# Kernel tuning notes

Measured on AMD Instinct MI355X. Metric: run time of the kernel, lower is better.

## Reference

```python
import jax, jax.numpy as jnp
import numpy as np
import math

D_MODEL = 1024
N_HEADS = 16
HEAD_DIM = D_MODEL // N_HEADS
THETA = 10000.0


def _rope(x, cos, sin):
    # x: [b, h, s, head_dim]; cos/sin: [s, head_dim//2]
    xe = x[..., 0::2]
    xo = x[..., 1::2]
    re = xe * cos - xo * sin
    ro = xe * sin + xo * cos
    # interleave back to even/odd layout
    return jnp.stack([re, ro], axis=-1).reshape(x.shape)


def setup_inputs() -> dict:
    key = jax.random.key(0)
    k1, k2, k3, k4, k5 = jax.random.split(key, 5)
    std = math.sqrt(2.0 / (D_MODEL + D_MODEL))
    x = jax.random.normal(k1, (2, 2048, D_MODEL), dtype=jnp.float32)
    Wq = jax.random.normal(k2, (D_MODEL, D_MODEL), dtype=jnp.float32) * std
    Wk = jax.random.normal(k3, (D_MODEL, D_MODEL), dtype=jnp.float32) * std
    Wv = jax.random.normal(k4, (D_MODEL, D_MODEL), dtype=jnp.float32) * std
    Wo = jax.random.normal(k5, (D_MODEL, D_MODEL), dtype=jnp.float32) * (std / math.sqrt(2))
    return {"x": x, "Wq": Wq, "Wk": Wk, "Wv": Wv, "Wo": Wo}


def reference(x, Wq, Wk, Wv, Wo):
    b, s, d = x.shape
    h, hd = N_HEADS, HEAD_DIM
    # projections: einsum 'batch seq d_in, d_model d_in -> batch seq d_model' == x @ W.T
    def proj(W):
        y = jnp.einsum('bsd,md->bsm', x, W)
        return y.reshape(b, s, h, hd).transpose(0, 2, 1, 3)  # [b, h, s, hd]
    Q, K, V = proj(Wq), proj(Wk), proj(Wv)
    # RoPE with default positions = arange(seq)
    freqs = 1.0 / (THETA ** (jnp.arange(0, hd, 2, dtype=jnp.float32) / hd))
    angles = jnp.arange(s, dtype=jnp.float32)[:, None] * freqs[None, :]  # [s, hd//2]
    cos, sin = jnp.cos(angles), jnp.sin(angles)
    Q = _rope(Q, cos, sin)
    K = _rope(K, cos, sin)
    # naive causal attention
    scores = jnp.einsum('bhqd,bhkd->bhqk', Q, K) / math.sqrt(hd)
    causal = jnp.tril(jnp.ones((s, s), dtype=bool))
    scores = jnp.where(causal, scores, -jnp.inf)
    attn = jax.nn.softmax(scores, axis=-1)
    out = jnp.einsum('bhqk,bhkd->bhqd', attn, V)
    out = out.transpose(0, 2, 1, 3).reshape(b, s, d)
    return jnp.einsum('bsd,md->bsm', out, Wo)
```

## Files before the change

### kernel.cpp

```cpp
#include <hip/hip_runtime.h>
#include <stdint.h>
#include <stddef.h>

typedef __bf16 bf16;
typedef __bf16 bf16x8 __attribute__((ext_vector_type(8)));
typedef __bf16 bf16x4 __attribute__((ext_vector_type(4)));
typedef short short4v __attribute__((ext_vector_type(4)));
typedef float f32x4 __attribute__((ext_vector_type(4)));

#define GAS __attribute__((address_space(1)))
#define LAS __attribute__((address_space(3)))

__device__ __forceinline__ void async_load16(const void* g, void* l) {
  __builtin_amdgcn_global_load_lds((const GAS void*)g, (LAS void*)l, 16, 0, 0);
}

__device__ __forceinline__ f32x4 mfma16(bf16x4 a, bf16x4 b, f32x4 c) {
#if defined(__HIP_DEVICE_COMPILE__)
#if __has_builtin(__builtin_amdgcn_mfma_f32_16x16x16bf16_1k)
  return __builtin_amdgcn_mfma_f32_16x16x16bf16_1k(
      __builtin_bit_cast(short4v, a), __builtin_bit_cast(short4v, b), c, 0, 0, 0);
#else
  f32x4 d;
  asm volatile("v_mfma_f32_16x16x16_bf16 %0, %1, %2, %3"
               : "=v"(d)
               : "v"(a), "v"(b), "v"(c));
  return d;
#endif
#else
  (void)a; (void)b;
  return c;
#endif
}

__global__ __launch_bounds__(256) void cast_all(
    const float* __restrict__ x, const float* __restrict__ Wq,
    const float* __restrict__ Wk, const float* __restrict__ Wv,
    const float* __restrict__ Wo, bf16* __restrict__ Xh,
    bf16* __restrict__ Wqkv, bf16* __restrict__ Woh,
    float2* __restrict__ rope) {
  if (blockIdx.x >= 8192) {
    const int e = ((blockIdx.x - 8192) * 256 + threadIdx.x) * 4;
    const int s = e >> 5, ip0 = e & 31;
#pragma unroll
    for (int r = 0; r < 4; ++r) {
      const float freq = __expf((float)(ip0 + r) * -0.2878231366242557f);
      float sn, cs;
      __sincosf((float)s * freq, &sn, &cs);
      rope[e + r] = make_float2(cs, sn);
    }
    return;
  }
  int idx = (blockIdx.x * 256 + threadIdx.x) * 4;
  const float* src;
  bf16* dst;
  float scale = 1.0f;
  if (idx < 4194304) {
    src = x + idx; dst = Xh + idx;
  } else if (idx < 7340032) {
    int j = idx - 4194304;
    if (j < 1048576) {
      src = Wq + j; scale = 0.18033688011112042f;
    } else {
      src = ((j < 2097152) ? Wk : Wv) + (j & 1048575);
    }
    dst = Wqkv + j;
  } else {
    int j = idx - 7340032;
    src = Wo + j; dst = Woh + j;
  }
  float4 v = *(const float4*)src;
  bf16x4 o;
  o[0] = (bf16)(v.x * scale); o[1] = (bf16)(v.y * scale);
  o[2] = (bf16)(v.z * scale); o[3] = (bf16)(v.w * scale);
  *(bf16x4*)dst = o;
}

__global__ __launch_bounds__(256, 3) void gemm_qkv(
    const bf16* __restrict__ A, const bf16* __restrict__ B,
    const float2* __restrict__ rope, bf16* __restrict__ Qh,
    bf16* __restrict__ Kh, bf16* __restrict__ Vt, int K) {
  __shared__ __align__(16) bf16 As[128 * 64];
  __shared__ __align__(16) bf16 Bs[128 * 64];
  const int tid = threadIdx.x;
  const int wave = tid >> 6, lane = tid & 63;
  const int bm = blockIdx.y * 128, bn = blockIdx.x * 128;
  const int wm = (wave >> 1) * 64, wn = (wave & 1) * 64;
  const int fr = lane & 15, g = lane >> 4;
  const int sw8 = (fr & 7) * 8;

  const int srow = tid >> 3;
  const int scol = 8 * ((tid & 7) ^ (srow & 7));
  const int ldst = wave * 512;

  f32x4 acc[4][4] = {};

  for (int kt = 0; kt < K; kt += 64) {
    __syncthreads();
#pragma unroll
    for (int s = 0; s < 4; ++s) {
      const int row = s * 32 + srow;
      async_load16(A + (size_t)(bm + row) * K + kt + scol,
                   (void*)(As + s * 2048 + ldst));
      async_load16(B + (size_t)(bn + row) * K + kt + scol,
                   (void*)(Bs + s * 2048 + ldst));
    }
    __syncthreads();

#pragma unroll
    for (int ks = 0; ks < 2; ++ks) {
      bf16x8 af[4], bfr[4];
      const int kq = (ks * 32 + g * 8) ^ sw8;
#pragma unroll
      for (int i = 0; i < 4; ++i)
        af[i] = *(const bf16x8*)&As[(wm + i * 16 + fr) * 64 + kq];
#pragma unroll
      for (int j = 0; j < 4; ++j)
        bfr[j] = *(const bf16x8*)&Bs[(wn + j * 16 + fr) * 64 + kq];
#pragma unroll
      for (int i = 0; i < 4; ++i)
#pragma unroll
        for (int j = 0; j < 4; ++j)
          acc[i][j] = __builtin_amdgcn_mfma_f32_16x16x32_bf16(af[i], bfr[j],
                                                              acc[i][j], 0, 0, 0);
    }
  }

  const int r0 = (lane >> 4) * 4, cc = lane & 15;
  const bool oddl = cc & 1;
#pragma unroll
  for (int i = 0; i < 4; ++i) {
    const int row0 = bm + wm + i * 16 + r0;
    const int b = row0 >> 11, s0 = row0 & 2047;
#pragma unroll
    for (int j = 0; j < 4; ++j) {
      const int col = bn + wn + j * 16 + cc;
      if (col < 2048) {
        const int hcol = col & 1023;
        const int h = hcol >> 6, d = hcol & 63;
        const int ip = d >> 1;
        const bool isK = col >= 1024;
        bf16* dst = (isK ? Kh : Qh) + ((size_t)(b * 16 + h) * 2048) * 64;
#pragma unroll
        for (int r = 0; r < 4; ++r) {
          float own = acc[i][j][r];
          float oth = __shfl_xor(own, 1, 64);
          const float2 t = rope[((s0 + r) << 5) + ip];
          float res = oddl ? (oth * t.y + own * t.x) : (own * t.x - oth * t.y);
          dst[(size_t)(s0 + r) * 64 + d] = (bf16)res;
        }
      } else {
        const int v = col - 2048, h = v >> 6, d = v & 63;
        bf16x4 o;
#pragma unroll
        for (int r = 0; r < 4; ++r) o[r] = (bf16)acc[i][j][r];
        const int s2 = (s0 & ~63) | ((s0 ^ ((d & 7) << 3)) & 63);
        *(bf16x4*)&Vt[(((size_t)b * 16 + h) * 64 + d) * 2048 + s2] = o;
      }
    }
  }
}

template <typename OutT, int BM, int BN>
__global__ __launch_bounds__(256) void gemm_bt(
    const bf16* __restrict__ A, const bf16* __restrict__ B,
    OutT* __restrict__ C, int M, int N, int K) {
  constexpr int FM = BM / 32, FN = BN / 32;
  constexpr int SA = BM / 32, SB = BN / 32;
  __shared__ __align__(16) bf16 As[BM * 64];
  __shared__ __align__(16) bf16 Bs[BN * 64];
  const int tid = threadIdx.x;
  const int wave = tid >> 6, lane = tid & 63;
  const int bm = blockIdx.y * BM, bn = blockIdx.x * BN;
  const int wm = (wave >> 1) * (BM / 2), wn = (wave & 1) * (BN / 2);
  const int fr = lane & 15, g = lane >> 4;
  const int sw8 = (fr & 7) * 8;
  const int srow = tid >> 3;
  const int scol = 8 * ((tid & 7) ^ (srow & 7));
  const int ldst = wave * 512;

  f32x4 acc[FM][FN] = {};

  for (int kt = 0; kt < K; kt += 64) {
    __syncthreads();
#pragma unroll
    for (int s = 0; s < SA; ++s)
      async_load16(A + (size_t)(bm + s * 32 + srow) * K + kt + scol,
                   (void*)(As + s * 2048 + ldst));
#pragma unroll
    for (int s = 0; s < SB; ++s)
      async_load16(B + (size_t)(bn + s * 32 + srow) * K + kt + scol,
                   (void*)(Bs + s * 2048 + ldst));
    __syncthreads();

#pragma unroll
    for (int ks = 0; ks < 2; ++ks) {
      const int kq = (ks * 32 + g * 8) ^ sw8;
      bf16x8 af[FM], bfr[FN];
#pragma unroll
      for (int i = 0; i < FM; ++i)
        af[i] = *(const bf16x8*)&As[(wm + i * 16 + fr) * 64 + kq];
#pragma unroll
      for (int j = 0; j < FN; ++j)
        bfr[j] = *(const bf16x8*)&Bs[(wn + j * 16 + fr) * 64 + kq];
#pragma unroll
      for (int i = 0; i < FM; ++i)
#pragma unroll
        for (int j = 0; j < FN; ++j)
          acc[i][j] = __builtin_amdgcn_mfma_f32_16x16x32_bf16(af[i], bfr[j],
                                                              acc[i][j], 0, 0, 0);
    }
  }

  const int r0 = (lane >> 4) * 4, cc = lane & 15;
#pragma unroll
  for (int i = 0; i < FM; ++i)
#pragma unroll
    for (int j = 0; j < FN; ++j)
#pragma unroll
      for (int r = 0; r < 4; ++r)
        C[(size_t)(bm + wm + i * 16 + r0 + r) * N + (bn + wn + j * 16 + cc)] =
            (OutT)acc[i][j][r];
}

__global__ __launch_bounds__(128, 2) void attn(const bf16* __restrict__ Qh,
                                               const bf16* __restrict__ Kh,
                                               const bf16* __restrict__ Vt,
                                               bf16* __restrict__ Oh) {
  __shared__ __align__(16) bf16 Vs[2][2][64 * 64];
  const int f = blockIdx.x;
  const int bh = f & 31;
  const int P = (f >> 5) & 31;
  const int tid = threadIdx.x, w = tid >> 6, lane = tid & 63;
  const int nlo = lane & 15, g = lane >> 4;
  const bf16* __restrict__ Qp = Qh + (size_t)bh * 131072;
  const bf16* __restrict__ Kp = Kh + (size_t)bh * 131072;
  const bf16* __restrict__ Vp = Vt + (size_t)bh * 131072;
  const int bb = bh >> 4, hd = bh & 15;
  const int sw = (nlo & 7) << 3;
  const int srow = lane >> 3, soff = (lane & 7) * 8;
  bf16* __restrict__ Vw0 = Vs[w][0];
  bf16* __restrict__ Vw1 = Vs[w][1];
  float* __restrict__ scr = (float*)Vs[1][0];
  float* __restrict__ scl = (float*)Vs[1][1];

  bf16x8 pkA[4][2], pkB[4][2];

  for (int ph = 0; ph < 2; ++ph) {
    const int qt = ph ? P : 63 - P;
    const int q0 = qt * 32;
    const int n = (qt >> 1) + 1;
    const int h = (n + 1) >> 1;
    const int t0 = w ? h : 0;
    const int cnt = w ? (n - h) : h;

    bf16x8 aq[2][2];
#pragma unroll
    for (int qb = 0; qb < 2; ++qb)
#pragma unroll
      for (int ks = 0; ks < 2; ++ks)
        aq[qb][ks] = *(const bf16x8*)&Qp[(size_t)(q0 + qb * 16 + nlo) * 64 +
                                         ks * 32 + g * 8];

    f32x4 oacc[2][4] = {};
    float lsum[2] = {0.f, 0.f};

    auto ldK = [&](bf16x8 (&pk)[4][2], int i) {
#pragma unroll
      for (int ni = 0; ni < 4; ++ni)
#pragma unroll
        for (int ks = 0; ks < 2; ++ks)
          pk[ni][ks] = *(const bf16x8*)&Kp[(size_t)(i * 64 + ni * 16 + nlo) * 64 +
                                           ks * 32 + g * 8];
    };
    auto stageV = [&](bf16* dst, int i) {
      const bf16* src = Vp + (size_t)srow * 2048 + i * 64 + soff;
#pragma unroll
      for (int c = 0; c < 8; ++c)
        async_load16(src + (size_t)c * 16384, (void*)(dst + c * 512));
    };

    auto body = [&](int it, bf16x8 (&pkC)[4][2], bf16x8 (&pkN)[4][2],
                    bf16* VwC, bf16* VwN) {
      const int i = t0 + it;
      asm volatile("s_waitcnt vmcnt(8)" ::: "memory");
      f32x4 st[2][4] = {};
#pragma unroll
      for (int qb = 0; qb < 2; ++qb)
#pragma unroll
        for (int ks = 0; ks < 2; ++ks)
#pragma unroll
          for (int ni = 0; ni < 4; ++ni)
            st[qb][ni] = __builtin_amdgcn_mfma_f32_16x16x32_bf16(
                pkC[ni][ks], aq[qb][ks], st[qb][ni], 0, 0, 0);
      const bool more = (it + 1 < cnt);
      if (more) {
        ldK(pkN, i + 1);
        stageV(VwN, i + 1);
      }
      const int kbase = i * 64;
      const bool dg = (i == n - 1);
      bf16x4 p[2][4];
#pragma unroll
      for (int qb = 0; qb < 2; ++qb) {
        const int qg = q0 + qb * 16 + nlo;
        if (!dg) {
#pragma unroll
          for (int ni = 0; ni < 4; ++ni)
#pragma unroll
            for (int r = 0; r < 4; ++r) {
              float e = __builtin_amdgcn_exp2f(st[qb][ni][r]);
              lsum[qb] += e;
              p[qb][ni][r] = (bf16)e;
            }
        } else {
#pragma unroll
          for (int ni = 0; ni < 4; ++ni) {
            const int kg0 = kbase + ni * 16 + g * 4;
#pragma unroll
            for (int r = 0; r < 4; ++r) {
              float e = __builtin_amdgcn_exp2f(st[qb][ni][r]);
              e = (kg0 + r <= qg) ? e : 0.0f;
              lsum[qb] += e;
              p[qb][ni][r] = (bf16)e;
            }
          }
        }
      }
      if (more)
        asm volatile("s_waitcnt vmcnt(16)" ::: "memory");
      else
        asm volatile("s_waitcnt vmcnt(0)" ::: "memory");
#pragma unroll
      for (int ni = 0; ni < 4; ++ni)
#pragma unroll
        for (int mi = 0; mi < 4; ++mi) {
          bf16x4 av = *(const bf16x4*)&VwC[(mi * 16 + nlo) * 64 +
                                           ((ni * 16 + g * 4) ^ sw)];
#pragma unroll
          for (int qb = 0; qb < 2; ++qb)
            oacc[qb][mi] = mfma16(av, p[qb][ni], oacc[qb][mi]);
        }
    };

    if (cnt > 0) {
      ldK(pkA, t0);
      stageV(Vw0, t0);
      int it = 0;
      while (true) {
        body(it, pkA, pkB, Vw0, Vw1);
        if (++it >= cnt) break;
        body(it, pkB, pkA, Vw1, Vw0);
        if (++it >= cnt) break;
      }
    }

#pragma unroll
    for (int qb = 0; qb < 2; ++qb) {
      lsum[qb] += __shfl_xor(lsum[qb], 16, 64);
      lsum[qb] += __shfl_xor(lsum[qb], 32, 64);
    }

    if (w == 1) {
#pragma unroll
      for (int qb = 0; qb < 2; ++qb) {
#pragma unroll
        for (int mi = 0; mi < 4; ++mi)
#pragma unroll
          for (int r = 0; r < 4; ++r)
            scr[(qb * 16 + mi * 4 + r) * 64 + lane] = oacc[qb][mi][r];
        scl[qb * 64 + lane] = lsum[qb];
      }
    }
    __syncthreads();
    if (w == 0) {
#pragma unroll
      for (int qb = 0; qb < 2; ++qb) {
        const float l = lsum[qb] + scl[qb * 64 + lane];
        const float inv = 1.0f / l;
        const int q = q0 + qb * 16 + nlo;
#pragma unroll
        for (int mi = 0; mi < 4; ++mi) {
          bf16x4 o;
#pragma unroll
          for (int r = 0; r < 4; ++r)
            o[r] = (bf16)((oacc[qb][mi][r] +
                           scr[(qb * 16 + mi * 4 + r) * 64 + lane]) * inv);
          *(bf16x4*)&Oh[((size_t)bb * 2048 + q) * 1024 + hd * 64 + mi * 16 +
                        g * 4] = o;
        }
      }
    }
    __syncthreads();
  }
}

extern "C" void kernel_launch(void* const* d_in, const int* in_sizes, int n_in,
                              void* d_out, int out_size, void* d_ws, size_t ws_size,
                              hipStream_t stream) {
  (void)in_sizes; (void)n_in; (void)out_size; (void)ws_size;
  const float* x = (const float*)d_in[0];
  const float* Wq = (const float*)d_in[1];
  const float* Wk = (const float*)d_in[2];
  const float* Wv = (const float*)d_in[3];
  const float* Wo = (const float*)d_in[4];
  float* out = (float*)d_out;
  char* ws = (char*)d_ws;

  bf16* Xh    = (bf16*)(ws);
  bf16* Wqkv  = (bf16*)(ws + 8388608);
  bf16* Woh   = (bf16*)(ws + 14680064);
  bf16* Qh    = (bf16*)(ws + 16777216);
  bf16* Kh    = (bf16*)(ws + 25165824);
  bf16* Vt    = (bf16*)(ws + 33554432);
  bf16* Oh    = (bf16*)(ws + 41943040);
  float2* rope = (float2*)(ws + 50331648);

  cast_all<<<8256, 256, 0, stream>>>(x, Wq, Wk, Wv, Wo, Xh, Wqkv, Woh, rope);
  gemm_qkv<<<dim3(24, 32), 256, 0, stream>>>(Xh, Wqkv, rope, Qh, Kh, Vt, 1024);
  attn<<<1024, 128, 0, stream>>>(Qh, Kh, Vt, Oh);
  gemm_bt<float, 128, 128><<<dim3(8, 32), 256, 0, stream>>>(Oh, Woh, out, 4096, 1024, 1024);
}
```

Measured before the change: 183.1 us.

## Software-pipeline attention loop: overlap PV of tile i with QK/exp of tile i+1

Restructures the per-wave KV loop into a skewed pipeline: each iteration runs the PV MFMAs for the current tile, issues the V stage for the next tile and a K prefetch two tiles ahead, then computes QK and exp for the next tile. This is meant to hide exp/VALU latency and load waits behind MFMA work, and it adds s_setprio around the MFMA blocks. It also adds a __syncthreads before the cross-wave reduction. The vmcnt accounting and the final V buffer selection are more intricate and could be fragile.

```diff
diff --git a/kernel.cpp b/kernel.cpp
--- a/kernel.cpp
+++ b/kernel.cpp
@@ -264,6 +264,8 @@
 
     f32x4 oacc[2][4] = {};
     float lsum[2] = {0.f, 0.f};
+    f32x4 st[2][4];
+    bf16x4 p[2][4];
 
     auto ldK = [&](bf16x8 (&pk)[4][2], int i) {
 #pragma unroll
@@ -279,28 +281,22 @@
       for (int c = 0; c < 8; ++c)
         async_load16(src + (size_t)c * 16384, (void*)(dst + c * 512));
     };
-
-    auto body = [&](int it, bf16x8 (&pkC)[4][2], bf16x8 (&pkN)[4][2],
-                    bf16* VwC, bf16* VwN) {
-      const int i = t0 + it;
-      asm volatile("s_waitcnt vmcnt(8)" ::: "memory");
-      f32x4 st[2][4] = {};
-#pragma unroll
-      for (int qb = 0; qb < 2; ++qb)
+    auto qk = [&](bf16x8 (&pk)[4][2]) {
+#pragma unroll
+      for (int qb = 0; qb < 2; ++qb) {
+#pragma unroll
+        for (int ni = 0; ni < 4; ++ni) st[qb][ni] = f32x4{0.f, 0.f, 0.f, 0.f};
 #pragma unroll
         for (int ks = 0; ks < 2; ++ks)
 #pragma unroll
           for (int ni = 0; ni < 4; ++ni)
             st[qb][ni] = __builtin_amdgcn_mfma_f32_16x16x32_bf16(
-                pkC[ni][ks], aq[qb][ks], st[qb][ni], 0, 0, 0);
-      const bool more = (it + 1 < cnt);
-      if (more) {
-        ldK(pkN, i + 1);
-        stageV(VwN, i + 1);
-      }
+                pk[ni][ks], aq[qb][ks], st[qb][ni], 0, 0, 0);
+      }
+    };
+    auto expv = [&](int i) {
       const int kbase = i * 64;
       const bool dg = (i == n - 1);
-      bf16x4 p[2][4];
 #pragma unroll
       for (int qb = 0; qb < 2; ++qb) {
         const int qg = q0 + qb * 16 + nlo;
@@ -327,32 +323,63 @@
           }
         }
       }
-      if (more)
-        asm volatile("s_waitcnt vmcnt(16)" ::: "memory");
-      else
-        asm volatile("s_waitcnt vmcnt(0)" ::: "memory");
+    };
+    auto pv = [&](const bf16* Vw) {
 #pragma unroll
       for (int ni = 0; ni < 4; ++ni)
 #pragma unroll
         for (int mi = 0; mi < 4; ++mi) {
-          bf16x4 av = *(const bf16x4*)&VwC[(mi * 16 + nlo) * 64 +
-                                           ((ni * 16 + g * 4) ^ sw)];
+          bf16x4 av = *(const bf16x4*)&Vw[(mi * 16 + nlo) * 64 +
+                                          ((ni * 16 + g * 4) ^ sw)];
 #pragma unroll
           for (int qb = 0; qb < 2; ++qb)
             oacc[qb][mi] = mfma16(av, p[qb][ni], oacc[qb][mi]);
         }
     };
 
+    auto body = [&](int it, bf16x8 (&pkQK)[4][2], bf16x8 (&pkPre)[4][2],
+                    bf16* VwC, bf16* VwN) {
+      const int i = t0 + it;
+      asm volatile("s_waitcnt vmcnt(8)" ::: "memory");
+      __builtin_amdgcn_s_setprio(1);
+      pv(VwC);
+      __builtin_amdgcn_s_setprio(0);
+      stageV(VwN, i + 1);
+      const bool preK = (it + 2 < cnt);
+      if (preK) ldK(pkPre, i + 2);
+      if (preK)
+        asm volatile("s_waitcnt vmcnt(16)" ::: "memory");
+      else
+        asm volatile("s_waitcnt vmcnt(8)" ::: "memory");
+      __builtin_amdgcn_s_setprio(1);
+      qk(pkQK);
+      __builtin_amdgcn_s_setprio(0);
+      expv(i + 1);
+    };
+
     if (cnt > 0) {
       ldK(pkA, t0);
       stageV(Vw0, t0);
+      if (cnt > 1) ldK(pkB, t0 + 1);
+      if (cnt > 1)
+        asm volatile("s_waitcnt vmcnt(16)" ::: "memory");
+      else
+        asm volatile("s_waitcnt vmcnt(8)" ::: "memory");
+      qk(pkA);
+      expv(t0);
+
       int it = 0;
-      while (true) {
-        body(it, pkA, pkB, Vw0, Vw1);
-        if (++it >= cnt) break;
-        body(it, pkB, pkA, Vw1, Vw0);
-        if (++it >= cnt) break;
-      }
+      while (it + 1 < cnt) {
+        body(it, pkB, pkA, Vw0, Vw1);
+        ++it;
+        if (it + 1 >= cnt) break;
+        body(it, pkA, pkB, Vw1, Vw0);
+        ++it;
+      }
+
+      asm volatile("s_waitcnt vmcnt(0)" ::: "memory");
+      pv((cnt & 1) ? ((cnt == 1) ? Vw0 : ((cnt - 1) & 1 ? Vw1 : Vw0))
+                   : Vw1);
     }
 
 #pragma unroll
@@ -361,6 +388,7 @@
       lsum[qb] += __shfl_xor(lsum[qb], 32, 64);
     }
 
+    __syncthreads();
     if (w == 1) {
 #pragma unroll
       for (int qb = 0; qb < 2; ++qb) {
```

New measurement: 204.0 us. +11.4%, slower.

## Single-buffer attention V staging and launch one query tile per block

Applied to the files above, without the earlier changes.

The attention kernel no longer pairs a long and a short query tile in one block. It launches 2048 blocks, one 32-row query tile each, ordered longest first. The V tile in LDS and the K register fragments are now single-buffered, which halves LDS per block, and launch bounds are raised to four blocks per SM. Prefetch of the next V tile only starts after the current tile's PV MFMAs, so less load latency is hidden per block; the design relies on higher occupancy to cover it.

```diff
diff --git a/kernel.cpp b/kernel.cpp
--- a/kernel.cpp
+++ b/kernel.cpp
@@ -223,175 +223,154 @@
             (OutT)acc[i][j][r];
 }
 
-__global__ __launch_bounds__(128, 2) void attn(const bf16* __restrict__ Qh,
+__global__ __launch_bounds__(128, 4) void attn(const bf16* __restrict__ Qh,
                                                const bf16* __restrict__ Kh,
                                                const bf16* __restrict__ Vt,
                                                bf16* __restrict__ Oh) {
-  __shared__ __align__(16) bf16 Vs[2][2][64 * 64];
+  __shared__ __align__(16) bf16 Vs[2][4096];
   const int f = blockIdx.x;
+  const int qt = 63 - (f >> 5);
   const int bh = f & 31;
-  const int P = (f >> 5) & 31;
   const int tid = threadIdx.x, w = tid >> 6, lane = tid & 63;
   const int nlo = lane & 15, g = lane >> 4;
+  const int q0 = qt * 32;
   const bf16* __restrict__ Qp = Qh + (size_t)bh * 131072;
   const bf16* __restrict__ Kp = Kh + (size_t)bh * 131072;
   const bf16* __restrict__ Vp = Vt + (size_t)bh * 131072;
+  const int n = (qt >> 1) + 1;
+  const int h = (n + 1) >> 1;
+  const int t0 = w ? h : 0;
+  const int cnt = w ? (n - h) : h;
   const int bb = bh >> 4, hd = bh & 15;
   const int sw = (nlo & 7) << 3;
   const int srow = lane >> 3, soff = (lane & 7) * 8;
-  bf16* __restrict__ Vw0 = Vs[w][0];
-  bf16* __restrict__ Vw1 = Vs[w][1];
-  float* __restrict__ scr = (float*)Vs[1][0];
-  float* __restrict__ scl = (float*)Vs[1][1];
-
-  bf16x8 pkA[4][2], pkB[4][2];
-
-  for (int ph = 0; ph < 2; ++ph) {
-    const int qt = ph ? P : 63 - P;
-    const int q0 = qt * 32;
-    const int n = (qt >> 1) + 1;
-    const int h = (n + 1) >> 1;
-    const int t0 = w ? h : 0;
-    const int cnt = w ? (n - h) : h;
-
-    bf16x8 aq[2][2];
-#pragma unroll
-    for (int qb = 0; qb < 2; ++qb)
+  bf16* __restrict__ Vw = Vs[w];
+
+  bf16x8 aq[2][2];
+#pragma unroll
+  for (int qb = 0; qb < 2; ++qb)
+#pragma unroll
+    for (int ks = 0; ks < 2; ++ks)
+      aq[qb][ks] = *(const bf16x8*)&Qp[(size_t)(q0 + qb * 16 + nlo) * 64 +
+                                       ks * 32 + g * 8];
+
+  f32x4 oacc[2][4] = {};
+  float lsum[2] = {0.f, 0.f};
+  bf16x8 pk[4][2];
+
+  auto ldK = [&](int i) {
+#pragma unroll
+    for (int ni = 0; ni < 4; ++ni)
 #pragma unroll
       for (int ks = 0; ks < 2; ++ks)
-        aq[qb][ks] = *(const bf16x8*)&Qp[(size_t)(q0 + qb * 16 + nlo) * 64 +
+        pk[ni][ks] = *(const bf16x8*)&Kp[(size_t)(i * 64 + ni * 16 + nlo) * 64 +
                                          ks * 32 + g * 8];
-
-    f32x4 oacc[2][4] = {};
-    float lsum[2] = {0.f, 0.f};
-
-    auto ldK = [&](bf16x8 (&pk)[4][2], int i) {
-#pragma unroll
-      for (int ni = 0; ni < 4; ++ni)
-#pragma unroll
-        for (int ks = 0; ks < 2; ++ks)
-          pk[ni][ks] = *(const bf16x8*)&Kp[(size_t)(i * 64 + ni * 16 + nlo) * 64 +
-                                           ks * 32 + g * 8];
-    };
-    auto stageV = [&](bf16* dst, int i) {
-      const bf16* src = Vp + (size_t)srow * 2048 + i * 64 + soff;
-#pragma unroll
-      for (int c = 0; c < 8; ++c)
-        async_load16(src + (size_t)c * 16384, (void*)(dst + c * 512));
-    };
-
-    auto body = [&](int it, bf16x8 (&pkC)[4][2], bf16x8 (&pkN)[4][2],
-                    bf16* VwC, bf16* VwN) {
-      const int i = t0 + it;
-      asm volatile("s_waitcnt vmcnt(8)" ::: "memory");
-      f32x4 st[2][4] = {};
-#pragma unroll
-      for (int qb = 0; qb < 2; ++qb)
-#pragma unroll
-        for (int ks = 0; ks < 2; ++ks)
-#pragma unroll
-          for (int ni = 0; ni < 4; ++ni)
-            st[qb][ni] = __builtin_amdgcn_mfma_f32_16x16x32_bf16(
-                pkC[ni][ks], aq[qb][ks], st[qb][ni], 0, 0, 0);
-      const bool more = (it + 1 < cnt);
-      if (more) {
-        ldK(pkN, i + 1);
-        stageV(VwN, i + 1);
-      }
-      const int kbase = i * 64;
-      const bool dg = (i == n - 1);
-      bf16x4 p[2][4];
-#pragma unroll
-      for (int qb = 0; qb < 2; ++qb) {
-        const int qg = q0 + qb * 16 + nlo;
-        if (!dg) {
-#pragma unroll
-          for (int ni = 0; ni < 4; ++ni)
-#pragma unroll
-            for (int r = 0; r < 4; ++r) {
-              float e = __builtin_amdgcn_exp2f(st[qb][ni][r]);
-              lsum[qb] += e;
-              p[qb][ni][r] = (bf16)e;
-            }
-        } else {
-#pragma unroll
-          for (int ni = 0; ni < 4; ++ni) {
-            const int kg0 = kbase + ni * 16 + g * 4;
-#pragma unroll
-            for (int r = 0; r < 4; ++r) {
-              float e = __builtin_amdgcn_exp2f(st[qb][ni][r]);
-              e = (kg0 + r <= qg) ? e : 0.0f;
-              lsum[qb] += e;
-              p[qb][ni][r] = (bf16)e;
-            }
+  };
+  auto stageV = [&](int i) {
+    const bf16* src = Vp + (size_t)srow * 2048 + i * 64 + soff;
+#pragma unroll
+    for (int c = 0; c < 8; ++c)
+      async_load16(src + (size_t)c * 16384, (void*)(Vw + c * 512));
+  };
+
+  if (cnt > 0) {
+    ldK(t0);
+    stageV(t0);
+  }
+
+  for (int it = 0; it < cnt; ++it) {
+    const int i = t0 + it, kbase = i * 64;
+    asm volatile("s_waitcnt vmcnt(0)" ::: "memory");
+    const bool dg = (i == n - 1);
+    bf16x4 p[2][4];
+#pragma unroll
+    for (int qb = 0; qb < 2; ++qb) {
+      f32x4 st[4] = {};
+#pragma unroll
+      for (int ks = 0; ks < 2; ++ks)
+#pragma unroll
+        for (int ni = 0; ni < 4; ++ni)
+          st[ni] = __builtin_amdgcn_mfma_f32_16x16x32_bf16(pk[ni][ks], aq[qb][ks],
+                                                           st[ni], 0, 0, 0);
+      const int qg = q0 + qb * 16 + nlo;
+      if (!dg) {
+#pragma unroll
+        for (int ni = 0; ni < 4; ++ni)
+#pragma unroll
+          for (int r = 0; r < 4; ++r) {
+            float e = __builtin_amdgcn_exp2f(st[ni][r]);
+            lsum[qb] += e;
+            p[qb][ni][r] = (bf16)e;
+          }
+      } else {
+#pragma unroll
+        for (int ni = 0; ni < 4; ++ni) {
+          const int kg0 = kbase + ni * 16 + g * 4;
+#pragma unroll
+          for (int r = 0; r < 4; ++r) {
+            float e = __builtin_amdgcn_exp2f(st[ni][r]);
+            e = (kg0 + r <= qg) ? e : 0.0f;
+            lsum[qb] += e;
+            p[qb][ni][r] = (bf16)e;
           }
         }
       }
-      if (more)
-        asm volatile("s_waitcnt vmcnt(16)" ::: "memory");
-      else
-        asm volatile("s_waitcnt vmcnt(0)" ::: "memory");
-#pragma unroll
-      for (int ni = 0; ni < 4; ++ni)
-#pragma unroll
-        for (int mi = 0; mi < 4; ++mi) {
-          bf16x4 av = *(const bf16x4*)&VwC[(mi * 16 + nlo) * 64 +
-                                           ((ni * 16 + g * 4) ^ sw)];
-#pragma unroll
-          for (int qb = 0; qb < 2; ++qb)
-            oacc[qb][mi] = mfma16(av, p[qb][ni], oacc[qb][mi]);
-        }
-    };
-
-    if (cnt > 0) {
-      ldK(pkA, t0);
-      stageV(Vw0, t0);
-      int it = 0;
-      while (true) {
-        body(it, pkA, pkB, Vw0, Vw1);
-        if (++it >= cnt) break;
-        body(it, pkB, pkA, Vw1, Vw0);
-        if (++it >= cnt) break;
+    }
+    if (it + 1 < cnt) ldK(i + 1);
+#pragma unroll
+    for (int ni = 0; ni < 4; ++ni)
+#pragma unroll
+      for (int mi = 0; mi < 4; ++mi) {
+        bf16x4 av = *(const bf16x4*)&Vw[(mi * 16 + nlo) * 64 +
+                                        ((ni * 16 + g * 4) ^ sw)];
+#pragma unroll
+        for (int qb = 0; qb < 2; ++qb)
+          oacc[qb][mi] = mfma16(av, p[qb][ni], oacc[qb][mi]);
       }
-    }
-
+    if (it + 1 < cnt) {
+      asm volatile("s_waitcnt lgkmcnt(0)" ::: "memory");
+      stageV(i + 1);
+    }
+  }
+
+#pragma unroll
+  for (int qb = 0; qb < 2; ++qb) {
+    lsum[qb] += __shfl_xor(lsum[qb], 16, 64);
+    lsum[qb] += __shfl_xor(lsum[qb], 32, 64);
+  }
+
+  float* __restrict__ scr = (float*)Vs[1];
+  float* __restrict__ scl = (float*)Vs[0];
+  __syncthreads();
+  if (w == 1) {
 #pragma unroll
     for (int qb = 0; qb < 2; ++qb) {
-      lsum[qb] += __shfl_xor(lsum[qb], 16, 64);
-      lsum[qb] += __shfl_xor(lsum[qb], 32, 64);
-    }
-
-    if (w == 1) {
-#pragma unroll
-      for (int qb = 0; qb < 2; ++qb) {
-#pragma unroll
-        for (int mi = 0; mi < 4; ++mi)
-#pragma unroll
-          for (int r = 0; r < 4; ++r)
-            scr[(qb * 16 + mi * 4 + r) * 64 + lane] = oacc[qb][mi][r];
-        scl[qb * 64 + lane] = lsum[qb];
+#pragma unroll
+      for (int mi = 0; mi < 4; ++mi)
+#pragma unroll
+        for (int r = 0; r < 4; ++r)
+          scr[(qb * 16 + mi * 4 + r) * 64 + lane] = oacc[qb][mi][r];
+      scl[qb * 64 + lane] = lsum[qb];
+    }
+  }
+  __syncthreads();
+  if (w == 0) {
+#pragma unroll
+    for (int qb = 0; qb < 2; ++qb) {
+      const float l = lsum[qb] + scl[qb * 64 + lane];
+      const float inv = 1.0f / l;
+      const int q = q0 + qb * 16 + nlo;
+#pragma unroll
+      for (int mi = 0; mi < 4; ++mi) {
+        bf16x4 o;
+#pragma unroll
+        for (int r = 0; r < 4; ++r)
+          o[r] = (bf16)((oacc[qb][mi][r] +
+                         scr[(qb * 16 + mi * 4 + r) * 64 + lane]) * inv);
+        *(bf16x4*)&Oh[((size_t)bb * 2048 + q) * 1024 + hd * 64 + mi * 16 +
+                      g * 4] = o;
       }
     }
-    __syncthreads();
-    if (w == 0) {
-#pragma unroll
-      for (int qb = 0; qb < 2; ++qb) {
-        const float l = lsum[qb] + scl[qb * 64 + lane];
-        const float inv = 1.0f / l;
-        const int q = q0 + qb * 16 + nlo;
-#pragma unroll
-        for (int mi = 0; mi < 4; ++mi) {
-          bf16x4 o;
-#pragma unroll
-          for (int r = 0; r < 4; ++r)
-            o[r] = (bf16)((oacc[qb][mi][r] +
-                           scr[(qb * 16 + mi * 4 + r) * 64 + lane]) * inv);
-          *(bf16x4*)&Oh[((size_t)bb * 2048 + q) * 1024 + hd * 64 + mi * 16 +
-                        g * 4] = o;
-        }
-      }
-    }
-    __syncthreads();
   }
 }
 
@@ -418,6 +397,6 @@
 
   cast_all<<<8256, 256, 0, stream>>>(x, Wq, Wk, Wv, Wo, Xh, Wqkv, Woh, rope);
   gemm_qkv<<<dim3(24, 32), 256, 0, stream>>>(Xh, Wqkv, rope, Qh, Kh, Vt, 1024);
-  attn<<<1024, 128, 0, stream>>>(Qh, Kh, Vt, Oh);
+  attn<<<2048, 128, 0, stream>>>(Qh, Kh, Vt, Oh);
   gemm_bt<float, 128, 128><<<dim3(8, 32), 256, 0, stream>>>(Oh, Woh, out, 4096, 1024, 1024);
 }
```

Result: slower. 212.1 us (+15.9%).
